# Performance work log

Measured on AMD Instinct MI355X. Metric: run time of the kernel, lower is better.

## Reference

```python
import jax, jax.numpy as jnp
import numpy as np

N_OBJ = 4096      # n_objects (fixed node count; fc1 consumes flattened node features)
F_IN = 256        # in_feats
H = 256           # n_hidden
C = 128           # n_classes
NE = 8            # number of edge types
EPT = 131072      # edges per etype (avg in-degree 32)


def setup_inputs() -> dict:
    key = jax.random.key(0)
    ks = jax.random.split(key, 16)
    s = 0.02  # weight init scale
    inp = {
        "feat": jax.random.normal(ks[0], (N_OBJ, F_IN), dtype=jnp.float32),
        "edges": jax.random.randint(ks[1], (NE, 2, EPT), 0, N_OBJ, dtype=jnp.int64),
        # 3 hetero layers: layer0 (F_IN->H), layers 1,2 (H->H), each with per-etype Linear
        "W0": jax.random.normal(ks[2], (NE, H, F_IN), dtype=jnp.float32) * s,
        "b0": jnp.zeros((NE, H), dtype=jnp.float32),
        "W1": jax.random.normal(ks[3], (NE, H, H), dtype=jnp.float32) * s,
        "b1": jnp.zeros((NE, H), dtype=jnp.float32),
        "W2": jax.random.normal(ks[4], (NE, H, H), dtype=jnp.float32) * s,
        "b2": jnp.zeros((NE, H), dtype=jnp.float32),
        "fc1_w": jax.random.normal(ks[5], (H, N_OBJ * H), dtype=jnp.float32) * 0.002,
        "fc1_b": jnp.zeros((H,), dtype=jnp.float32),
        "fc2_w": jax.random.normal(ks[6], (C, H), dtype=jnp.float32) * s,
        "fc2_b": jnp.zeros((C,), dtype=jnp.float32),
    }
    return inp


def _hetero_layer(h, W, b, edges):
    # Per-etype linear: Wh[e] = h @ W[e].T + b[e]   -> [NE, N, H]
    Wh = jnp.einsum('nf,ehf->enh', h, W) + b[:, None, :]

    def per_etype(wh, src, dst):
        msg = wh[src]                                            # gather: [EPT, H]
        ssum = jax.ops.segment_sum(msg, dst, num_segments=N_OBJ)  # [N, H]
        deg = jax.ops.segment_sum(jnp.ones_like(dst, dtype=wh.dtype), dst,
                                  num_segments=N_OBJ)             # [N]
        return ssum / jnp.maximum(deg, 1.0)[:, None]              # mean reduce

    agg = jax.vmap(per_etype)(Wh, edges[:, 0], edges[:, 1])  # [NE, N, H]
    # multi_update_all cross-type aggregator 'sum', then activation (relu)
    return jax.nn.relu(agg.sum(axis=0))


def reference(feat, edges, W0, b0, W1, b1, W2, b2, fc1_w, fc1_b, fc2_w, fc2_b):
    h = _hetero_layer(feat, W0, b0, edges)
    h = _hetero_layer(h, W1, b1, edges)
    h = _hetero_layer(h, W2, b2, edges)
    flat = h.reshape(-1)                          # [N*H]
    z = jax.nn.relu(fc1_w @ flat + fc1_b)         # [H]
    out = jax.nn.sigmoid(fc2_w @ z + fc2_b)       # [C]
    return out
```

## Files before the change

kernel.cpp:

```cpp
#include <hip/hip_runtime.h>
#include <math.h>

#define N_OBJ 4096
#define F     256
#define NE    8
#define EPT   131072
#define KCAT  (NE * F)
#define C_OUT 128
#define FC1_K (N_OBJ * F)
#define FCH   16384
#define FNCH  (FC1_K / FCH)
#define FRJ   8

typedef __attribute__((ext_vector_type(8))) short s8v;
typedef __attribute__((ext_vector_type(4))) float f4v;

__device__ inline float bf2f(unsigned short u) {
    unsigned int x = ((unsigned int)u) << 16;
    return __builtin_bit_cast(float, x);
}
__device__ inline unsigned short f2bf(float f) {
    unsigned int x = __builtin_bit_cast(unsigned int, f);
    x += 0x7fff + ((x >> 16) & 1);
    return (unsigned short)(x >> 16);
}
__device__ __forceinline__ int swz(int row, int k8) {
    return (row * 64 + k8 * 8) ^ ((row & 7) << 3);
}


__global__ __launch_bounds__(256) void k_count_deg(const int* __restrict__ edges,
                                                   int* __restrict__ deg) {
    int gid = blockIdx.x * 256 + threadIdx.x;
    int e = gid >> 17;
    int i = gid & (EPT - 1);
    int dst = edges[(e * 2 + 1) * EPT + i];
    atomicAdd(&deg[e * N_OBJ + dst], 1);
}

__global__ __launch_bounds__(256) void k_scan(const int* __restrict__ deg,
                                              int* __restrict__ rowptr,
                                              int* __restrict__ cursor,
                                              float* __restrict__ invdeg) {
    int e = blockIdx.x;
    int t = threadIdx.x;
    __shared__ int part[256];
    int local[16];
    int base = e * N_OBJ + t * 16;
    int s = 0;
#pragma unroll
    for (int i = 0; i < 16; ++i) { local[i] = deg[base + i]; s += local[i]; }
    part[t] = s;
    __syncthreads();
    for (int off = 1; off < 256; off <<= 1) {
        int v = (t >= off) ? part[t - off] : 0;
        __syncthreads();
        part[t] += v;
        __syncthreads();
    }
    int run = part[t] - s;
#pragma unroll
    for (int i = 0; i < 16; ++i) {
        rowptr[base + i] = run;
        cursor[base + i] = run;
        invdeg[base + i] = 1.0f / fmaxf((float)local[i], 1.0f);
        run += local[i];
    }
}

__global__ __launch_bounds__(256) void k_fill(const int* __restrict__ edges,
                                              int* __restrict__ cursor,
                                              int* __restrict__ col) {
    int gid = blockIdx.x * 256 + threadIdx.x;
    int e = gid >> 17;
    int i = gid & (EPT - 1);
    int src = edges[(e * 2 + 0) * EPT + i];
    int dst = edges[(e * 2 + 1) * EPT + i];
    int pos = atomicAdd(&cursor[e * N_OBJ + dst], 1);
    col[e * EPT + pos] = src;
}

__global__ __launch_bounds__(256) void k_bmask(const int* __restrict__ deg,
                                               unsigned int* __restrict__ bmask) {
    int n = blockIdx.x * 256 + threadIdx.x;
    unsigned int m = 0;
#pragma unroll
    for (int e = 0; e < NE; ++e) m |= (deg[e * N_OBJ + n] > 0) ? (1u << e) : 0u;
    bmask[n] = m;
}

#define WQ4 (NE * F * F / 4)
#define FQ4 (N_OBJ * F / 4)
__global__ __launch_bounds__(256) void k_cvt_all(const float* __restrict__ W0,
                                                 const float* __restrict__ W1,
                                                 const float* __restrict__ W2,
                                                 const float* __restrict__ feat,
                                                 unsigned short* __restrict__ Wb0,
                                                 unsigned short* __restrict__ Wb1,
                                                 unsigned short* __restrict__ Wb2,
                                                 unsigned short* __restrict__ featb) {
    int i = blockIdx.x * 256 + threadIdx.x;
    const float* s;
    unsigned short* d;
    int j;
    if (i < WQ4)            { s = W0;   d = Wb0;   j = i; }
    else if (i < 2 * WQ4)   { s = W1;   d = Wb1;   j = i - WQ4; }
    else if (i < 3 * WQ4)   { s = W2;   d = Wb2;   j = i - 2 * WQ4; }
    else                    { s = feat; d = featb; j = i - 3 * WQ4; }
    float4 v = ((const float4*)s)[j];
    ushort4 o;
    o.x = f2bf(v.x); o.y = f2bf(v.y); o.z = f2bf(v.z); o.w = f2bf(v.w);
    ((ushort4*)d)[j] = o;
}

__global__ __launch_bounds__(256) void k_aggregate(const unsigned short* __restrict__ h_in,
                                                   const int* __restrict__ rowptr,
                                                   const int* __restrict__ deg,
                                                   const int* __restrict__ col,
                                                   const float* __restrict__ invdeg,
                                                   unsigned short* __restrict__ ah) {
    int wid = blockIdx.x * 4 + (threadIdx.x >> 6);
    int lane = threadIdx.x & 63;
    int e = wid >> 12;
    int n = wid & (N_OBJ - 1);
    int beg = rowptr[wid];
    int cnt = deg[wid];
    const int* cl = col + e * EPT + beg;
    const ushort4* h4 = (const ushort4*)h_in;
    float a0 = 0.f, a1 = 0.f, a2 = 0.f, a3 = 0.f;
    int k = 0;
    for (; k + 8 <= cnt; k += 8) {
        int s0 = cl[k],     s1 = cl[k + 1], s2 = cl[k + 2], s3 = cl[k + 3];
        int s4 = cl[k + 4], s5 = cl[k + 5], s6 = cl[k + 6], s7 = cl[k + 7];
        ushort4 v0 = h4[s0 * 64 + lane];
        ushort4 v1 = h4[s1 * 64 + lane];
        ushort4 v2 = h4[s2 * 64 + lane];
        ushort4 v3 = h4[s3 * 64 + lane];
        ushort4 v4 = h4[s4 * 64 + lane];
        ushort4 v5 = h4[s5 * 64 + lane];
        ushort4 v6 = h4[s6 * 64 + lane];
        ushort4 v7 = h4[s7 * 64 + lane];
        a0 += bf2f(v0.x) + bf2f(v1.x) + bf2f(v2.x) + bf2f(v3.x)
            + bf2f(v4.x) + bf2f(v5.x) + bf2f(v6.x) + bf2f(v7.x);
        a1 += bf2f(v0.y) + bf2f(v1.y) + bf2f(v2.y) + bf2f(v3.y)
            + bf2f(v4.y) + bf2f(v5.y) + bf2f(v6.y) + bf2f(v7.y);
        a2 += bf2f(v0.z) + bf2f(v1.z) + bf2f(v2.z) + bf2f(v3.z)
            + bf2f(v4.z) + bf2f(v5.z) + bf2f(v6.z) + bf2f(v7.z);
        a3 += bf2f(v0.w) + bf2f(v1.w) + bf2f(v2.w) + bf2f(v3.w)
            + bf2f(v4.w) + bf2f(v5.w) + bf2f(v6.w) + bf2f(v7.w);
    }
    for (; k < cnt; ++k) {
        ushort4 v = h4[cl[k] * 64 + lane];
        a0 += bf2f(v.x); a1 += bf2f(v.y); a2 += bf2f(v.z); a3 += bf2f(v.w);
    }
    float sc = invdeg[wid];
    ushort4 o;
    o.x = f2bf(a0 * sc); o.y = f2bf(a1 * sc); o.z = f2bf(a2 * sc); o.w = f2bf(a3 * sc);
    ((ushort4*)ah)[n * (KCAT / 4) + e * (F / 4) + lane] = o;
}

template <int OUTBF>
__global__ __launch_bounds__(256, 4) void k_gemm(const unsigned short* __restrict__ A,
                                                 const unsigned short* __restrict__ Wb,
                                                 const float* __restrict__ bias,
                                                 const unsigned int* __restrict__ bmask,
                                                 void* __restrict__ Cout) {
    __shared__ short As[2][64 * 64];
    __shared__ short Bs[2][64 * 64];
    int m0 = blockIdx.x * 64, n0 = blockIdx.y * 64;
    int t = threadIdx.x;
    int wave = t >> 6, lane = t & 63;
    int r = lane & 15, g = lane >> 4;
    int row0 = t >> 3, seg0 = t & 7;
    int row1 = row0 + 32;
    int wA0 = swz(row0, seg0), wA1 = swz(row1, seg0);

    const short* Ap = (const short*)A;
    const short* Wp = (const short*)Wb;
    const short* arp0 = Ap + (size_t)(m0 + row0) * KCAT + seg0 * 8;
    const short* arp1 = Ap + (size_t)(m0 + row1) * KCAT + seg0 * 8;
    int brow0 = (n0 + row0) * F + seg0 * 8;
    int brow1 = (n0 + row1) * F + seg0 * 8;

    f4v acc[4];
#pragma unroll
    for (int i = 0; i < 4; ++i) acc[i] = (f4v){0.f, 0.f, 0.f, 0.f};

    {
        s8v a0 = *(const s8v*)(arp0);
        s8v a1 = *(const s8v*)(arp1);
        s8v b0 = *(const s8v*)(Wp + brow0);
        s8v b1 = *(const s8v*)(Wp + brow1);
        *(s8v*)&As[0][wA0] = a0; *(s8v*)&As[0][wA1] = a1;
        *(s8v*)&Bs[0][wA0] = b0; *(s8v*)&Bs[0][wA1] = b1;
    }
    __syncthreads();
#pragma unroll 1
    for (int ks = 0; ks < 32; ++ks) {
        int cur = ks & 1;
        s8v a0, a1, b0, b1;
        if (ks < 31) {
            int kb = (ks + 1) * 64;
            int woff = ((kb >> 8) << 16) + (kb & 255);
            a0 = *(const s8v*)(arp0 + kb);
            a1 = *(const s8v*)(arp1 + kb);
            b0 = *(const s8v*)(Wp + woff + brow0);
            b1 = *(const s8v*)(Wp + woff + brow1);
        }
        const short* as = As[cur];
        const short* bs = Bs[cur];
#pragma unroll
        for (int kk = 0; kk < 2; ++kk) {
            s8v af = *(const s8v*)&as[swz(wave * 16 + r, kk * 4 + g)];
#pragma unroll
            for (int n = 0; n < 4; ++n) {
                s8v bf = *(const s8v*)&bs[swz(n * 16 + r, kk * 4 + g)];
                acc[n] = __builtin_amdgcn_mfma_f32_16x16x32_bf16(af, bf, acc[n], 0, 0, 0);
            }
        }
        if (ks < 31) {
            *(s8v*)&As[cur ^ 1][wA0] = a0; *(s8v*)&As[cur ^ 1][wA1] = a1;
            *(s8v*)&Bs[cur ^ 1][wA0] = b0; *(s8v*)&Bs[cur ^ 1][wA1] = b1;
        }
        __syncthreads();
    }
    int mb = m0 + wave * 16 + g * 4;
    unsigned int msk[4];
#pragma unroll
    for (int reg = 0; reg < 4; ++reg) msk[reg] = bmask[mb + reg];
#pragma unroll
    for (int n = 0; n < 4; ++n) {
        int coln = n0 + n * 16 + r;
        float bcol[NE];
#pragma unroll
        for (int e = 0; e < NE; ++e) bcol[e] = bias[e * F + coln];
#pragma unroll
        for (int reg = 0; reg < 4; ++reg) {
            float v = acc[n][reg];
#pragma unroll
            for (int e = 0; e < NE; ++e)
                if ((msk[reg] >> e) & 1) v += bcol[e];
            v = fmaxf(v, 0.f);
            if (OUTBF) ((unsigned short*)Cout)[(size_t)(mb + reg) * F + coln] = f2bf(v);
            else       ((float*)Cout)[(size_t)(mb + reg) * F + coln] = v;
        }
    }
}

__global__ __launch_bounds__(256) void k_fc1(const float* __restrict__ Wf,
                                             const float* __restrict__ flat,
                                             float* __restrict__ zpart) {
    __shared__ float xs[FCH];
    int c = blockIdx.x;
    int jg = blockIdx.y;
    int t = threadIdx.x;
    const float4* fp = (const float4*)(flat + (size_t)c * FCH);
    float4* xs4 = (float4*)xs;
#pragma unroll
    for (int q = 0; q < FCH / 4 / 256; ++q) xs4[q * 256 + t] = fp[q * 256 + t];
    __syncthreads();
    float accs[FRJ];
#pragma unroll
    for (int rr = 0; rr < FRJ; ++rr) {
        const float4* wp = (const float4*)(Wf + (size_t)(jg * FRJ + rr) * FC1_K
                                              + (size_t)c * FCH);
        float s = 0.0f;
#pragma unroll 4
        for (int it = 0; it < FCH / 4 / 256; ++it) {
            int q = it * 256 + t;
            float4 w4 = wp[q];
            float4 x4 = xs4[q];
            s = fmaf(w4.x, x4.x,
                fmaf(w4.y, x4.y,
                fmaf(w4.z, x4.z,
                fmaf(w4.w, x4.w, s))));
        }
        accs[rr] = s;
    }
    __shared__ float red[4][FRJ];
    int lane = t & 63, wv = t >> 6;
#pragma unroll
    for (int rr = 0; rr < FRJ; ++rr) {
        float s = accs[rr];
#pragma unroll
        for (int off = 32; off > 0; off >>= 1) s += __shfl_down(s, off, 64);
        if (lane == 0) red[wv][rr] = s;
    }
    __syncthreads();
    if (t < FRJ) {
        float s = red[0][t] + red[1][t] + red[2][t] + red[3][t];
        zpart[c * 256 + jg * FRJ + t] = s;
    }
}

__global__ __launch_bounds__(256) void k_final(const float* __restrict__ zpart,
                                               const float* __restrict__ fc1_b,
                                               const float* __restrict__ fc2_w,
                                               const float* __restrict__ fc2_b,
                                               float* __restrict__ out) {
    __shared__ float z[256];
    int t = threadIdx.x;
    float s = fc1_b[t];
#pragma unroll
    for (int c = 0; c < FNCH; ++c) s += zpart[c * 256 + t];
    z[t] = fmaxf(s, 0.0f);
    __syncthreads();
    if (t < C_OUT) {
        float acc = fc2_b[t];
        for (int k = 0; k < 256; ++k) acc = fmaf(fc2_w[t * 256 + k], z[k], acc);
        out[t] = 1.0f / (1.0f + expf(-acc));
    }
}

extern "C" void kernel_launch(void* const* d_in, const int* in_sizes, int n_in,
                              void* d_out, int out_size, void* d_ws, size_t ws_size,
                              hipStream_t stream) {
    const float* feat  = (const float*)d_in[0];
    const int*   edges = (const int*)d_in[1];
    const float* W0    = (const float*)d_in[2];
    const float* b0    = (const float*)d_in[3];
    const float* W1    = (const float*)d_in[4];
    const float* b1    = (const float*)d_in[5];
    const float* W2    = (const float*)d_in[6];
    const float* b2    = (const float*)d_in[7];
    const float* fc1_w = (const float*)d_in[8];
    const float* fc1_b = (const float*)d_in[9];
    const float* fc2_w = (const float*)d_in[10];
    const float* fc2_b = (const float*)d_in[11];
    float* out = (float*)d_out;

    char* ws = (char*)d_ws;
    size_t off = 0;
    auto alloc = [&](size_t bytes) {
        void* p = ws + off;
        off = (off + bytes + 255) & ~(size_t)255;
        return p;
    };
    int*            deg    = (int*)            alloc(NE * N_OBJ * 4);
    int*            rowptr = (int*)            alloc(NE * N_OBJ * 4);
    int*            cursor = (int*)            alloc(NE * N_OBJ * 4);
    float*          invdeg = (float*)          alloc(NE * N_OBJ * 4);
    int*            col    = (int*)            alloc(NE * EPT * 4);
    unsigned int*   bmask  = (unsigned int*)   alloc(N_OBJ * 4);
    float*          zpart  = (float*)          alloc(FNCH * 256 * 4);
    unsigned short* Wb0    = (unsigned short*) alloc((size_t)NE * F * F * 2);
    unsigned short* Wb1    = (unsigned short*) alloc((size_t)NE * F * F * 2);
    unsigned short* Wb2    = (unsigned short*) alloc((size_t)NE * F * F * 2);
    unsigned short* featb  = (unsigned short*) alloc((size_t)N_OBJ * F * 2);
    unsigned short* h_ba   = (unsigned short*) alloc((size_t)N_OBJ * F * 2);
    unsigned short* h_bb   = (unsigned short*) alloc((size_t)N_OBJ * F * 2);
    float*          h_f32  = (float*)          alloc((size_t)N_OBJ * F * 4);
    unsigned short* ah     = (unsigned short*) alloc((size_t)N_OBJ * KCAT * 2);
    (void)ws_size; (void)in_sizes; (void)n_in; (void)out_size;

    hipMemsetAsync(deg, 0, NE * N_OBJ * 4, stream);
    k_count_deg<<<NE * EPT / 256, 256, 0, stream>>>(edges, deg);
    k_scan<<<NE, 256, 0, stream>>>(deg, rowptr, cursor, invdeg);
    k_fill<<<NE * EPT / 256, 256, 0, stream>>>(edges, cursor, col);
    k_bmask<<<N_OBJ / 256, 256, 0, stream>>>(deg, bmask);
    k_cvt_all<<<(3 * WQ4 + FQ4) / 256, 256, 0, stream>>>(W0, W1, W2, feat,
                                                         Wb0, Wb1, Wb2, featb);

    dim3 ggrid(N_OBJ / 64, F / 64);
    int agrid = NE * N_OBJ / 4;

    k_aggregate<<<agrid, 256, 0, stream>>>(featb, rowptr, deg, col, invdeg, ah);
    k_gemm<1><<<ggrid, 256, 0, stream>>>(ah, Wb0, b0, bmask, h_ba);
    k_aggregate<<<agrid, 256, 0, stream>>>(h_ba, rowptr, deg, col, invdeg, ah);
    k_gemm<1><<<ggrid, 256, 0, stream>>>(ah, Wb1, b1, bmask, h_bb);
    k_aggregate<<<agrid, 256, 0, stream>>>(h_bb, rowptr, deg, col, invdeg, ah);
    k_gemm<0><<<ggrid, 256, 0, stream>>>(ah, Wb2, b2, bmask, h_f32);

    dim3 fgrid(FNCH, 256 / FRJ);
    k_fc1<<<fgrid, 256, 0, stream>>>(fc1_w, h_f32, zpart);
    k_final<<<1, 256, 0, stream>>>(zpart, fc1_b, fc2_w, fc2_b, out);
}
```

Before: 484.8 us.

## Fold bmask into scan, unroll GEMM double-buffer, restructure fc1 with register-held inputs

The bmask kernel is removed and the mask is built with atomicOr inside the scan kernel. Its buffer is placed next to deg so a single memset clears both, which saves one launch. The GEMM main loop is unrolled by two with separate register sets, so global loads for step k+2 are issued before compute on step k, hiding more load latency at the cost of extra registers. The fc1 kernel keeps its input chunk in registers instead of LDS and handles 32 rows per block instead of 8. This cuts the grid and redundant reloads of the input chunk, but each block runs a long serial loop over rows and uses more registers.

```diff
diff --git a/kernel.cpp b/kernel.cpp
--- a/kernel.cpp
+++ b/kernel.cpp
@@ -10,7 +10,7 @@
 #define FC1_K (N_OBJ * F)
 #define FCH   16384
 #define FNCH  (FC1_K / FCH)
-#define FRJ   8
+#define FRJ   32
 
 typedef __attribute__((ext_vector_type(8))) short s8v;
 typedef __attribute__((ext_vector_type(4))) float f4v;
@@ -41,7 +41,8 @@
 __global__ __launch_bounds__(256) void k_scan(const int* __restrict__ deg,
                                               int* __restrict__ rowptr,
                                               int* __restrict__ cursor,
-                                              float* __restrict__ invdeg) {
+                                              float* __restrict__ invdeg,
+                                              unsigned int* __restrict__ bmask) {
     int e = blockIdx.x;
     int t = threadIdx.x;
     __shared__ int part[256];
@@ -64,6 +65,7 @@
         rowptr[base + i] = run;
         cursor[base + i] = run;
         invdeg[base + i] = 1.0f / fmaxf((float)local[i], 1.0f);
+        if (local[i] > 0) atomicOr(&bmask[t * 16 + i], 1u << e);
         run += local[i];
     }
 }
@@ -78,15 +80,6 @@
     int dst = edges[(e * 2 + 1) * EPT + i];
     int pos = atomicAdd(&cursor[e * N_OBJ + dst], 1);
     col[e * EPT + pos] = src;
-}
-
-__global__ __launch_bounds__(256) void k_bmask(const int* __restrict__ deg,
-                                               unsigned int* __restrict__ bmask) {
-    int n = blockIdx.x * 256 + threadIdx.x;
-    unsigned int m = 0;
-#pragma unroll
-    for (int e = 0; e < NE; ++e) m |= (deg[e * N_OBJ + n] > 0) ? (1u << e) : 0u;
-    bmask[n] = m;
 }
 
 #define WQ4 (NE * F * F / 4)
@@ -159,6 +152,19 @@
     ((ushort4*)ah)[n * (KCAT / 4) + e * (F / 4) + lane] = o;
 }
 
+#define GEMM_COMPUTE(as, bs)                                                            \
+    {                                                                                   \
+        _Pragma("unroll")                                                               \
+        for (int kk = 0; kk < 2; ++kk) {                                                \
+            s8v af = *(const s8v*)&as[swz(wave * 16 + r, kk * 4 + g)];                  \
+            _Pragma("unroll")                                                           \
+            for (int n = 0; n < 4; ++n) {                                               \
+                s8v bf = *(const s8v*)&bs[swz(n * 16 + r, kk * 4 + g)];                 \
+                acc[n] = __builtin_amdgcn_mfma_f32_16x16x32_bf16(af, bf, acc[n], 0,0,0);\
+            }                                                                           \
+        }                                                                               \
+    }
+
 template <int OUTBF>
 __global__ __launch_bounds__(256, 4) void k_gemm(const unsigned short* __restrict__ A,
                                                  const unsigned short* __restrict__ Wb,
@@ -194,33 +200,39 @@
         *(s8v*)&As[0][wA0] = a0; *(s8v*)&As[0][wA1] = a1;
         *(s8v*)&Bs[0][wA0] = b0; *(s8v*)&Bs[0][wA1] = b1;
     }
+    s8v rAa0, rAa1, rAb0, rAb1, rBa0, rBa1, rBb0, rBb1;
+    {
+        int kb = 64, woff = ((kb >> 8) << 16) + (kb & 255);
+        rAa0 = *(const s8v*)(arp0 + kb);
+        rAa1 = *(const s8v*)(arp1 + kb);
+        rAb0 = *(const s8v*)(Wp + woff + brow0);
+        rAb1 = *(const s8v*)(Wp + woff + brow1);
+    }
     __syncthreads();
 #pragma unroll 1
-    for (int ks = 0; ks < 32; ++ks) {
-        int cur = ks & 1;
-        s8v a0, a1, b0, b1;
-        if (ks < 31) {
-            int kb = (ks + 1) * 64;
-            int woff = ((kb >> 8) << 16) + (kb & 255);
-            a0 = *(const s8v*)(arp0 + kb);
-            a1 = *(const s8v*)(arp1 + kb);
-            b0 = *(const s8v*)(Wp + woff + brow0);
-            b1 = *(const s8v*)(Wp + woff + brow1);
-        }
-        const short* as = As[cur];
-        const short* bs = Bs[cur];
-#pragma unroll
-        for (int kk = 0; kk < 2; ++kk) {
-            s8v af = *(const s8v*)&as[swz(wave * 16 + r, kk * 4 + g)];
-#pragma unroll
-            for (int n = 0; n < 4; ++n) {
-                s8v bf = *(const s8v*)&bs[swz(n * 16 + r, kk * 4 + g)];
-                acc[n] = __builtin_amdgcn_mfma_f32_16x16x32_bf16(af, bf, acc[n], 0, 0, 0);
-            }
-        }
-        if (ks < 31) {
-            *(s8v*)&As[cur ^ 1][wA0] = a0; *(s8v*)&As[cur ^ 1][wA1] = a1;
-            *(s8v*)&Bs[cur ^ 1][wA0] = b0; *(s8v*)&Bs[cur ^ 1][wA1] = b1;
+    for (int i = 0; i < 16; ++i) {
+        if (i < 15) {
+            int kb = (2 * i + 2) * 64, woff = ((kb >> 8) << 16) + (kb & 255);
+            rBa0 = *(const s8v*)(arp0 + kb);
+            rBa1 = *(const s8v*)(arp1 + kb);
+            rBb0 = *(const s8v*)(Wp + woff + brow0);
+            rBb1 = *(const s8v*)(Wp + woff + brow1);
+        }
+        GEMM_COMPUTE(As[0], Bs[0]);
+        *(s8v*)&As[1][wA0] = rAa0; *(s8v*)&As[1][wA1] = rAa1;
+        *(s8v*)&Bs[1][wA0] = rAb0; *(s8v*)&Bs[1][wA1] = rAb1;
+        __syncthreads();
+        if (i < 15) {
+            int kb = (2 * i + 3) * 64, woff = ((kb >> 8) << 16) + (kb & 255);
+            rAa0 = *(const s8v*)(arp0 + kb);
+            rAa1 = *(const s8v*)(arp1 + kb);
+            rAb0 = *(const s8v*)(Wp + woff + brow0);
+            rAb1 = *(const s8v*)(Wp + woff + brow1);
+        }
+        GEMM_COMPUTE(As[1], Bs[1]);
+        if (i < 15) {
+            *(s8v*)&As[0][wA0] = rBa0; *(s8v*)&As[0][wA1] = rBa1;
+            *(s8v*)&Bs[0][wA0] = rBb0; *(s8v*)&Bs[0][wA1] = rBb1;
         }
         __syncthreads();
     }
@@ -250,46 +262,39 @@
 __global__ __launch_bounds__(256) void k_fc1(const float* __restrict__ Wf,
                                              const float* __restrict__ flat,
                                              float* __restrict__ zpart) {
-    __shared__ float xs[FCH];
+    __shared__ float part[FRJ][260];
     int c = blockIdx.x;
     int jg = blockIdx.y;
     int t = threadIdx.x;
     const float4* fp = (const float4*)(flat + (size_t)c * FCH);
-    float4* xs4 = (float4*)xs;
-#pragma unroll
-    for (int q = 0; q < FCH / 4 / 256; ++q) xs4[q * 256 + t] = fp[q * 256 + t];
+    float4 xr[16];
+#pragma unroll
+    for (int q = 0; q < 16; ++q) xr[q] = fp[q * 256 + t];
+    const float* wbase = Wf + (size_t)(jg * FRJ) * FC1_K + (size_t)c * FCH;
+#pragma unroll 1
+    for (int rr = 0; rr < FRJ; ++rr) {
+        const float4* wp = (const float4*)(wbase + (size_t)rr * FC1_K);
+        float s = 0.0f;
+#pragma unroll
+        for (int it = 0; it < 16; ++it) {
+            float4 w4 = wp[it * 256 + t];
+            s = fmaf(w4.x, xr[it].x,
+                fmaf(w4.y, xr[it].y,
+                fmaf(w4.z, xr[it].z,
+                fmaf(w4.w, xr[it].w, s))));
+        }
+        part[rr][t] = s;
+    }
     __syncthreads();
-    float accs[FRJ];
-#pragma unroll
-    for (int rr = 0; rr < FRJ; ++rr) {
-        const float4* wp = (const float4*)(Wf + (size_t)(jg * FRJ + rr) * FC1_K
-                                              + (size_t)c * FCH);
-        float s = 0.0f;
-#pragma unroll 4
-        for (int it = 0; it < FCH / 4 / 256; ++it) {
-            int q = it * 256 + t;
-            float4 w4 = wp[q];
-            float4 x4 = xs4[q];
-            s = fmaf(w4.x, x4.x,
-                fmaf(w4.y, x4.y,
-                fmaf(w4.z, x4.z,
-                fmaf(w4.w, x4.w, s))));
-        }
-        accs[rr] = s;
-    }
-    __shared__ float red[4][FRJ];
-    int lane = t & 63, wv = t >> 6;
-#pragma unroll
-    for (int rr = 0; rr < FRJ; ++rr) {
-        float s = accs[rr];
+    int wv = t >> 6, lane = t & 63;
+#pragma unroll
+    for (int q = 0; q < 8; ++q) {
+        int rr = wv * 8 + q;
+        float s = part[rr][lane] + part[rr][lane + 64]
+                + part[rr][lane + 128] + part[rr][lane + 192];
 #pragma unroll
         for (int off = 32; off > 0; off >>= 1) s += __shfl_down(s, off, 64);
-        if (lane == 0) red[wv][rr] = s;
-    }
-    __syncthreads();
-    if (t < FRJ) {
-        float s = red[0][t] + red[1][t] + red[2][t] + red[3][t];
-        zpart[c * 256 + jg * FRJ + t] = s;
+        if (lane == 0) zpart[c * 256 + jg * FRJ + rr] = s;
     }
 }
 
@@ -337,11 +342,11 @@
         return p;
     };
     int*            deg    = (int*)            alloc(NE * N_OBJ * 4);
+    unsigned int*   bmask  = (unsigned int*)   alloc(N_OBJ * 4);
     int*            rowptr = (int*)            alloc(NE * N_OBJ * 4);
     int*            cursor = (int*)            alloc(NE * N_OBJ * 4);
     float*          invdeg = (float*)          alloc(NE * N_OBJ * 4);
     int*            col    = (int*)            alloc(NE * EPT * 4);
-    unsigned int*   bmask  = (unsigned int*)   alloc(N_OBJ * 4);
     float*          zpart  = (float*)          alloc(FNCH * 256 * 4);
     unsigned short* Wb0    = (unsigned short*) alloc((size_t)NE * F * F * 2);
     unsigned short* Wb1    = (unsigned short*) alloc((size_t)NE * F * F * 2);
@@ -353,11 +358,10 @@
     unsigned short* ah     = (unsigned short*) alloc((size_t)N_OBJ * KCAT * 2);
     (void)ws_size; (void)in_sizes; (void)n_in; (void)out_size;
 
-    hipMemsetAsync(deg, 0, NE * N_OBJ * 4, stream);
+    hipMemsetAsync(deg, 0, NE * N_OBJ * 4 + N_OBJ * 4, stream);
     k_count_deg<<<NE * EPT / 256, 256, 0, stream>>>(edges, deg);
-    k_scan<<<NE, 256, 0, stream>>>(deg, rowptr, cursor, invdeg);
+    k_scan<<<NE, 256, 0, stream>>>(deg, rowptr, cursor, invdeg, bmask);
     k_fill<<<NE * EPT / 256, 256, 0, stream>>>(edges, cursor, col);
-    k_bmask<<<N_OBJ / 256, 256, 0, stream>>>(deg, bmask);
     k_cvt_all<<<(3 * WQ4 + FQ4) / 256, 256, 0, stream>>>(W0, W1, W2, feat,
                                                          Wb0, Wb1, Wb2, featb);
 
```

Result: slower. 523.6 us (+8.0%).
